# Kernel optimization log

Hardware: AMD Instinct MI355X
Metric: run time of the kernel (lower is better)

Reference implementation:

```python
import jax, jax.numpy as jnp
import numpy as np

B, S, K = 256, 50, 8
D, NH, NL = 512, 8, 2
N_KNOWS, N_PROBS = 1000, 20000
L2 = 2 * NL  # forward layers then backward layers, stacked
HD = D // NH
NEG = -1e9


def _ln(x, g, b, eps=1e-5):
    mu = x.mean(-1, keepdims=True)
    v = ((x - mu) ** 2).mean(-1, keepdims=True)
    return (x - mu) * jax.lax.rsqrt(v + eps) * g + b


def _block(x, m, Wq, bq, Wk, bk, Wv, bv, g1, be1, W1, b1, W2, b2, g2, be2):
    # x: [3B,S,D], m: [3B,1,S,S] additive-OR mask (True = blocked)
    Bx, Sx, Dx = x.shape
    Q = (x @ Wq + bq).reshape(Bx, Sx, NH, HD)
    Kt = (x @ Wk + bk).reshape(Bx, Sx, NH, HD)
    V = (x @ Wv + bv).reshape(Bx, Sx, NH, HD)
    a = jnp.einsum('bqnh,bknh->bnqk', Q, Kt) * (HD ** -0.5)
    a = jnp.where(m, NEG, a)
    p = jax.nn.softmax(a, axis=-1)
    p = jnp.where(m, 0.0, p)  # masked_fill + softmax + where, as in torch source
    o = jnp.einsum('bnqk,bknh->bqnh', p, V).reshape(Bx, Sx, Dx)
    x = _ln(x + o, g1, be1)
    h = jnp.maximum(x @ W1 + b1, 0.0) @ W2 + b2
    return _ln(x + h, g2, be2)


def _forward(probs_his, knows_his, corrs_his, knows_tab, probs_tab, types_tab, pos_tab,
             Wq, bq, Wk, bk, Wv, bv, g1, be1, W1, b1, W2, b2, g2, be2,
             pW1, pb1, pW2, pb2, pW3, pb3):
    info = knows_tab[knows_his].sum(-2) + probs_tab[probs_his] + pos_tab[jnp.arange(S)][None]
    c = corrs_his
    right_t = jnp.where(c, 1, 2)   # corrs==False -> 2
    wrong_t = jnp.where(c, 2, 0)   # corrs==True  -> 2
    norm_t = c.astype(jnp.int32)
    # fold the 3 counterfactual passes (right / wrong / normal) into the batch dim
    x3 = jnp.concatenate([info + types_tab[right_t], info + types_tab[wrong_t], info + types_tab[norm_t]], 0)
    kpm = jnp.tile(probs_his == 0, (3, 1))               # key padding mask [3B,S]
    km = kpm[:, :, None] | kpm[:, None, :]               # OR-combined [3B,S,S]
    tri = jnp.triu(jnp.ones((S, S), bool), 1)
    fm = (tri[None] | km)[:, None]                       # forward (causal) mask
    bm = (tri.T[None] | km)[:, None]                     # backward (anti-causal) mask
    f = x3
    b = x3
    for i in range(NL):
        f = _block(f, fm, Wq[i], bq[i], Wk[i], bk[i], Wv[i], bv[i], g1[i], be1[i], W1[i], b1[i], W2[i], b2[i], g2[i], be2[i])
    for i in range(NL, L2):
        b = _block(b, bm, Wq[i], bq[i], Wk[i], bk[i], Wv[i], bv[i], g1[i], be1[i], W1[i], b1[i], W2[i], b2[i], g2[i], be2[i])
    out = jnp.concatenate([b[:, :1], f[:, :-2] + b[:, 2:], f[:, -1:]], 1)
    h = jnp.concatenate([out, jnp.tile(info, (3, 1, 1))], -1)
    h = jnp.maximum(h @ pW1 + pb1, 0.0)
    h = jnp.maximum(h @ pW2 + pb2, 0.0)
    sc = jax.nn.sigmoid((h @ pW3 + pb3)[..., 0]).reshape(3, B, S)
    # zero out padded positions instead of ragged boolean gather (fixed shape, jit-safe)
    return jnp.where((probs_his > 0)[None], sc, 0.0)


def setup_inputs() -> dict:
    key = jax.random.key(0)
    ks = jax.random.split(key, 16)
    sc = 0.02
    d = {}
    d['probs_his'] = jax.random.randint(ks[0], (B, S), 0, N_PROBS)
    d['knows_his'] = jax.random.randint(ks[1], (B, S, K), 0, N_KNOWS + 1)
    d['corrs_his'] = jax.random.randint(ks[2], (B, S), 0, 2).astype(bool)
    d['knows_tab'] = (jax.random.normal(ks[3], (N_KNOWS + 1, D)) * sc).at[0].set(0.0)  # padding_idx=0
    d['probs_tab'] = (jax.random.normal(ks[4], (N_PROBS + 1, D)) * sc).at[0].set(0.0)
    d['types_tab'] = jax.random.normal(ks[5], (3, D)) * sc
    d['pos_tab'] = jax.random.normal(ks[6], (50, D)) * sc
    d['Wq'] = jax.random.normal(ks[7], (L2, D, D)) * sc
    d['Wk'] = jax.random.normal(ks[8], (L2, D, D)) * sc
    d['Wv'] = jax.random.normal(ks[9], (L2, D, D)) * sc
    d['W1'] = jax.random.normal(ks[10], (L2, D, D)) * sc
    d['W2'] = jax.random.normal(ks[11], (L2, D, D)) * sc
    for n in ('bq', 'bk', 'bv', 'b1', 'b2', 'be1', 'be2'):
        d[n] = jnp.zeros((L2, D))
    d['g1'] = jnp.ones((L2, D))
    d['g2'] = jnp.ones((L2, D))
    d['pW1'] = jax.random.normal(ks[12], (2 * D, D)) * sc
    d['pb1'] = jnp.zeros((D,))
    d['pW2'] = jax.random.normal(ks[13], (D, D // 2)) * sc
    d['pb2'] = jnp.zeros((D // 2,))
    d['pW3'] = jax.random.normal(ks[14], (D // 2, 1)) * sc
    d['pb3'] = jnp.zeros((1,))
    return d


def reference(probs_his, knows_his, corrs_his, knows_tab, probs_tab, types_tab, pos_tab,
              Wq, bq, Wk, bk, Wv, bv, g1, be1, W1, b1, W2, b2, g2, be2,
              pW1, pb1, pW2, pb2, pW3, pb3):
    return _forward(probs_his, knows_his, corrs_his, knows_tab, probs_tab, types_tab, pos_tab,
                    Wq, bq, Wk, bk, Wv, bv, g1, be1, W1, b1, W2, b2, g2, be2,
                    pW1, pb1, pW2, pb2, pW3, pb3)
```

## Files before the change

kernel.cpp:

```cpp
#include <hip/hip_runtime.h>
#include <hip/hip_bf16.h>

#define SEQ 50
#define DD  512
#define NHD 8
#define HDIM 64
#define MPROWS 38400
#define MTROWS 76800

typedef __hip_bfloat16 bf;
typedef __attribute__((ext_vector_type(8))) short bf16x8;
typedef __attribute__((ext_vector_type(4))) float f32x4;

__device__ __forceinline__ float bf2f(unsigned short u) {
    unsigned int x = ((unsigned int)u) << 16;
    return __builtin_bit_cast(float, x);
}
__device__ __forceinline__ unsigned short f2bu(float f) {
    unsigned int u = __builtin_bit_cast(unsigned int, f);
    u += 0x7fffu + ((u >> 16) & 1u);
    return (unsigned short)(u >> 16);
}

#define ASYNC16(g, l) __builtin_amdgcn_global_load_lds( \
    (__attribute__((address_space(1))) void*)(g),       \
    (__attribute__((address_space(3))) void*)(l), 16, 0, 0)

__global__ __launch_bounds__(256) void transpose_cast(
    const float* __restrict__ src, bf* __restrict__ dst,
    int R, int C, size_t sStride, size_t dStride)
{
    __shared__ float tile[32][33];
    int l = blockIdx.z;
    src += (size_t)l * sStride;
    dst += (size_t)l * dStride;
    int c0 = blockIdx.x * 32, r0 = blockIdx.y * 32;
    int tx = threadIdx.x & 31, ty = threadIdx.x >> 5;
    for (int i = ty; i < 32; i += 8)
        tile[i][tx] = src[(size_t)(r0 + i) * C + c0 + tx];
    __syncthreads();
    for (int i = ty; i < 32; i += 8)
        dst[(size_t)(c0 + i) * R + r0 + tx] = __float2bfloat16(tile[tx][i]);
}

__global__ __launch_bounds__(256) void biascat_kernel(
    const float* __restrict__ bq, const float* __restrict__ bk,
    const float* __restrict__ bv, float* __restrict__ out)
{
    int i = blockIdx.x * 256 + threadIdx.x;
    if (i >= 4 * 1536) return;
    int l = i / 1536, c = i % 1536;
    float v;
    if (c < 512)       v = bq[l * 512 + c];
    else if (c < 1024) v = bk[l * 512 + c - 512];
    else               v = bv[l * 512 + c - 1024];
    out[i] = v;
}

__global__ __launch_bounds__(256) void tproj_kernel(
    const float* __restrict__ types_tab, const bf* __restrict__ WTqkv,
    bf* __restrict__ Tt)
{
    int gid = blockIdx.x * 256 + threadIdx.x;
    if (gid >= 9216) return;
    int hl = gid / 4608;
    int t  = (gid / 1536) % 3;
    int n  = gid % 1536;
    const unsigned short* w =
        (const unsigned short*)(WTqkv + (size_t)(hl * 2) * 786432 + (size_t)n * 512);
    const float* ty = types_tab + t * 512;
    float a = 0.f;
    for (int k = 0; k < 512; ++k) a += ty[k] * bf2f(w[k]);
    Tt[gid] = __float2bfloat16(a);
}

__global__ __launch_bounds__(256) void embed_kernel(
    const int* __restrict__ probs_his, const int* __restrict__ knows_his,
    const int* __restrict__ corrs, const float* __restrict__ knows_tab,
    const float* __restrict__ probs_tab, const float* __restrict__ types_tab,
    const float* __restrict__ pos_tab, bf* __restrict__ info, bf* __restrict__ X)
{
    int bs = blockIdx.x * 4 + (threadIdx.x >> 6);
    int lane = threadIdx.x & 63;
    int s = bs % SEQ;
    int p = probs_his[bs];
    int c = corrs[bs];
    int d0 = lane * 8;

    float v[8];
    #pragma unroll
    for (int j = 0; j < 8; ++j)
        v[j] = probs_tab[(size_t)p * DD + d0 + j] + pos_tab[(size_t)s * DD + d0 + j];
    for (int k = 0; k < 8; ++k) {
        int ki = knows_his[bs * 8 + k];
        const float* kr = knows_tab + (size_t)ki * DD + d0;
        #pragma unroll
        for (int j = 0; j < 8; ++j) v[j] += kr[j];
    }
    int t0 = c ? 1 : 2;
    int t1 = c ? 2 : 0;
    int t2 = c ? 1 : 0;
    const float* T0 = types_tab + t0 * DD + d0;
    const float* T1 = types_tab + t1 * DD + d0;
    const float* T2 = types_tab + t2 * DD + d0;
    uint4 xi, x0, x1, x2;
    unsigned short* pi = (unsigned short*)&xi;
    unsigned short* p0 = (unsigned short*)&x0;
    unsigned short* p1 = (unsigned short*)&x1;
    unsigned short* p2 = (unsigned short*)&x2;
    #pragma unroll
    for (int j = 0; j < 8; ++j) {
        pi[j] = f2bu(v[j]);
        p0[j] = f2bu(v[j] + T0[j]);
        p1[j] = f2bu(v[j] + T1[j]);
        p2[j] = f2bu(v[j] + T2[j]);
    }
    size_t base = (size_t)bs * DD + d0;
    const size_t PB = (size_t)12800 * DD;
    *(uint4*)(info + base) = xi;
    *(uint4*)(X + 0 * PB + base) = x0;
    *(uint4*)(X + 1 * PB + base) = x1;
    *(uint4*)(X + 2 * PB + base) = x2;
    *(uint4*)(X + 3 * PB + base) = x0;
    *(uint4*)(X + 4 * PB + base) = x1;
    *(uint4*)(X + 5 * PB + base) = x2;
}

template <int RELU>
__global__ __launch_bounds__(256) void gemm_bt(
    const bf* __restrict__ Ap, const bf* __restrict__ WT0, const bf* __restrict__ WT1,
    const float* __restrict__ bias0, const float* __restrict__ bias1,
    bf* __restrict__ Cp, int N, int Kd, int nN, int mtHalf)
{
    __shared__ bf Al[128 * 64];
    __shared__ bf Bl[128 * 64];
    int nwg = gridDim.x;
    int f = blockIdx.x;
    int q8 = nwg >> 3, r8 = nwg & 7;
    int xcd = f & 7, pos = f >> 3;
    int e = (xcd < r8 ? xcd * (q8 + 1) : r8 * (q8 + 1) + (xcd - r8) * q8) + pos;
    int bm = e / nN, bn = e - bm * nN;
    const bf* WTp;
    const float* bias;
    if (bm < mtHalf) { WTp = WT0; bias = bias0; }
    else             { WTp = WT1; bias = bias1; }
    int m0 = bm * 128, n0 = bn * 128;
    int t = threadIdx.x, lane = t & 63, wave = t >> 6;
    int wr = wave >> 1, wc = wave & 1;
    int lr = lane & 15, lg = lane >> 4;

    f32x4 acc[4][4];
    #pragma unroll
    for (int m = 0; m < 4; ++m)
        #pragma unroll
        for (int n = 0; n < 4; ++n)
            acc[m][n] = (f32x4){0.f, 0.f, 0.f, 0.f};

    for (int kt = 0; kt < Kd; kt += 64) {
        #pragma unroll
        for (int i = 0; i < 4; ++i) {
            int c = i * 256 + t;
            int row = c >> 3, col = (c & 7) * 8;
            ASYNC16(Ap  + (size_t)(m0 + row) * Kd + kt + col, Al + c * 8);
            ASYNC16(WTp + (size_t)(n0 + row) * Kd + kt + col, Bl + c * 8);
        }
        __syncthreads();
        #pragma unroll
        for (int kk = 0; kk < 64; kk += 32) {
            int ko = kk + lg * 8;
            bf16x8 af[4], bfr[4];
            #pragma unroll
            for (int m = 0; m < 4; ++m)
                af[m] = *(const bf16x8*)(Al + (wr * 64 + m * 16 + lr) * 64 + ko);
            #pragma unroll
            for (int n = 0; n < 4; ++n)
                bfr[n] = *(const bf16x8*)(Bl + (wc * 64 + n * 16 + lr) * 64 + ko);
            #pragma unroll
            for (int m = 0; m < 4; ++m)
                #pragma unroll
                for (int n = 0; n < 4; ++n)
                    acc[m][n] = __builtin_amdgcn_mfma_f32_16x16x32_bf16(af[m], bfr[n], acc[m][n], 0, 0, 0);
        }
        __syncthreads();
    }
    unsigned short* Cs = (unsigned short*)Cp;
    #pragma unroll
    for (int n = 0; n < 4; ++n) {
        int col = n0 + wc * 64 + n * 16 + lr;
        float bvv = bias[col];
        #pragma unroll
        for (int m = 0; m < 4; ++m) {
            #pragma unroll
            for (int r = 0; r < 4; ++r) {
                int row = m0 + wr * 64 + m * 16 + lg * 4 + r;
                float v = acc[m][n][r] + bvv;
                if (RELU) v = fmaxf(v, 0.f);
                Cs[(size_t)row * N + col] = f2bu(v);
            }
        }
    }
}

template <int RELU>
__global__ __launch_bounds__(512, 2) void gemm8(
    const bf* __restrict__ Ap, const bf* __restrict__ WTp,
    const float* __restrict__ bias, bf* __restrict__ Cp,
    int N, int Kd, int nN)
{
    __shared__ __align__(16) bf As[2][16384];
    __shared__ __align__(16) bf Bs[2][16384];

    int nwg = gridDim.x, f = blockIdx.x;
    int q8 = nwg >> 3, r8 = nwg & 7;
    int xcd = f & 7, pos = f >> 3;
    int e = (xcd < r8 ? xcd * (q8 + 1) : r8 * (q8 + 1) + (xcd - r8) * q8) + pos;
    int bm = e / nN, bn = e - bm * nN;
    int m0 = bm * 256, n0 = bn * 256;
    int t = threadIdx.x, lane = t & 63, wave = t >> 6;
    int wm = wave >> 2, wn = wave & 3;
    int lr = lane & 15, kg = lane >> 4;

    int srow = t >> 3;
    int scolb = (t & 7) * 16;
    const bf* Abase = Ap + (size_t)m0 * Kd;
    const bf* Bbase = WTp + (size_t)n0 * Kd;

#define STG(dsts, base, half, kt) do {                                        \
    _Pragma("unroll")                                                         \
    for (int _i = 0; _i < 2; ++_i) {                                          \
        int _r = (half) * 128 + _i * 64 + srow;                               \
        ASYNC16((base) + (size_t)_r * Kd + (kt) +                             \
                    ((scolb ^ ((_r & 7) << 4)) >> 1),                         \
                (dsts) + _r * 64 + (t & 7) * 8);                              \
    } } while (0)

    f32x4 acc[8][4];
    #pragma unroll
    for (int m = 0; m < 8; ++m)
        #pragma unroll
        for (int n = 0; n < 4; ++n)
            acc[m][n] = (f32x4){0.f, 0.f, 0.f, 0.f};

    STG(As[0], Abase, 0, 0);
    STG(As[0], Abase, 1, 0);
    STG(Bs[0], Bbase, 0, 0);
    STG(Bs[0], Bbase, 1, 0);

    int ntile = Kd >> 6;
    bf16x8 breg[4][2];
    for (int j = 0; j < ntile; ++j) {
        int d = j & 1;
        const char* Ab = (const char*)As[d];
        const char* Bb = (const char*)Bs[d];
        asm volatile("s_waitcnt vmcnt(0)" ::: "memory");
        __builtin_amdgcn_s_barrier();
        int kt1 = (j + 1) << 6;
        int pf = (j + 1 < ntile);
        #pragma unroll
        for (int q = 0; q < 4; ++q) {
            if (q == 0) {
                #pragma unroll
                for (int ns = 0; ns < 4; ++ns) {
                    int row = wn * 64 + ns * 16 + lr;
                    int sw = (row & 7) << 4;
                    breg[ns][0] = *(const bf16x8*)(Bb + row * 128 + ((kg * 16) ^ sw));
                    breg[ns][1] = *(const bf16x8*)(Bb + row * 128 + ((64 + kg * 16) ^ sw));
                }
            }
            bf16x8 areg[2][2];
            #pragma unroll
            for (int mm = 0; mm < 2; ++mm) {
                int row = wm * 128 + (2 * q + mm) * 16 + lr;
                int sw = (row & 7) << 4;
                areg[mm][0] = *(const bf16x8*)(Ab + row * 128 + ((kg * 16) ^ sw));
                areg[mm][1] = *(const bf16x8*)(Ab + row * 128 + ((64 + kg * 16) ^ sw));
            }
            if (pf) {
                if (q == 0)      STG(As[d ^ 1], Abase, 0, kt1);
                else if (q == 1) STG(As[d ^ 1], Abase, 1, kt1);
                else if (q == 2) STG(Bs[d ^ 1], Bbase, 0, kt1);
                else             STG(Bs[d ^ 1], Bbase, 1, kt1);
            }
            __builtin_amdgcn_s_barrier();
            __builtin_amdgcn_s_setprio(1);
            #pragma unroll
            for (int mm = 0; mm < 2; ++mm)
                #pragma unroll
                for (int ns = 0; ns < 4; ++ns) {
                    acc[2 * q + mm][ns] = __builtin_amdgcn_mfma_f32_16x16x32_bf16(
                        areg[mm][0], breg[ns][0], acc[2 * q + mm][ns], 0, 0, 0);
                    acc[2 * q + mm][ns] = __builtin_amdgcn_mfma_f32_16x16x32_bf16(
                        areg[mm][1], breg[ns][1], acc[2 * q + mm][ns], 0, 0, 0);
                }
            __builtin_amdgcn_s_setprio(0);
            if (q != 3) __builtin_amdgcn_s_barrier();
        }
    }
#undef STG

    unsigned short* Cs = (unsigned short*)Cp;
    #pragma unroll
    for (int ns = 0; ns < 4; ++ns) {
        int col = n0 + wn * 64 + ns * 16 + lr;
        float bvv = bias[col];
        #pragma unroll
        for (int ms = 0; ms < 8; ++ms) {
            #pragma unroll
            for (int rr = 0; rr < 4; ++rr) {
                int row = m0 + wm * 128 + ms * 16 + kg * 4 + rr;
                float v = acc[ms][ns][rr] + bvv;
                if (RELU) v = fmaxf(v, 0.f);
                Cs[(size_t)row * N + col] = f2bu(v);
            }
        }
    }
}

__global__ __launch_bounds__(256) void gemm_l0(
    const bf* __restrict__ Ap, const bf* __restrict__ WTp,
    const float* __restrict__ bias, const bf* __restrict__ Tth,
    const int* __restrict__ corrs, bf* __restrict__ QKVc)
{
    __shared__ bf Al[128 * 64];
    __shared__ bf Bl[128 * 64];
    const int nN = 12, Kd = 512, N = 1536;
    int nwg = gridDim.x;
    int f = blockIdx.x;
    int q8 = nwg >> 3, r8 = nwg & 7;
    int xcd = f & 7, pos = f >> 3;
    int e = (xcd < r8 ? xcd * (q8 + 1) : r8 * (q8 + 1) + (xcd - r8) * q8) + pos;
    int bm = e / nN, bn = e - bm * nN;
    int m0 = bm * 128, n0 = bn * 128;
    int t = threadIdx.x, lane = t & 63, wave = t >> 6;
    int wr = wave >> 1, wc = wave & 1;
    int lr = lane & 15, lg = lane >> 4;

    f32x4 acc[4][4];
    #pragma unroll
    for (int m = 0; m < 4; ++m)
        #pragma unroll
        for (int n = 0; n < 4; ++n)
            acc[m][n] = (f32x4){0.f, 0.f, 0.f, 0.f};

    for (int kt = 0; kt < Kd; kt += 64) {
        #pragma unroll
        for (int i = 0; i < 4; ++i) {
            int c = i * 256 + t;
            int row = c >> 3, col = (c & 7) * 8;
            ASYNC16(Ap  + (size_t)(m0 + row) * Kd + kt + col, Al + c * 8);
            ASYNC16(WTp + (size_t)(n0 + row) * Kd + kt + col, Bl + c * 8);
        }
        __syncthreads();
        #pragma unroll
        for (int kk = 0; kk < 64; kk += 32) {
            int ko = kk + lg * 8;
            bf16x8 af[4], bfr[4];
            #pragma unroll
            for (int m = 0; m < 4; ++m)
                af[m] = *(const bf16x8*)(Al + (wr * 64 + m * 16 + lr) * 64 + ko);
            #pragma unroll
            for (int n = 0; n < 4; ++n)
                bfr[n] = *(const bf16x8*)(Bl + (wc * 64 + n * 16 + lr) * 64 + ko);
            #pragma unroll
            for (int m = 0; m < 4; ++m)
                #pragma unroll
                for (int n = 0; n < 4; ++n)
                    acc[m][n] = __builtin_amdgcn_mfma_f32_16x16x32_bf16(af[m], bfr[n], acc[m][n], 0, 0, 0);
        }
        __syncthreads();
    }
    unsigned short* Cs = (unsigned short*)QKVc;
    const unsigned short* Tu = (const unsigned short*)Tth;
    #pragma unroll
    for (int n = 0; n < 4; ++n) {
        int col = n0 + wc * 64 + n * 16 + lr;
        float bvv = bias[col];
        float T0c = bf2f(Tu[0 * 1536 + col]);
        float T1c = bf2f(Tu[1 * 1536 + col]);
        float T2c = bf2f(Tu[2 * 1536 + col]);
        #pragma unroll
        for (int m = 0; m < 4; ++m) {
            #pragma unroll
            for (int r = 0; r < 4; ++r) {
                int row = m0 + wr * 64 + m * 16 + lg * 4 + r;
                int c = corrs[row];
                float v = acc[m][n][r] + bvv;
                float tv0 = c ? T1c : T2c;
                float tv1 = c ? T2c : T0c;
                float tv2 = c ? T1c : T0c;
                size_t b0 = (size_t)row * N + col;
                Cs[b0]                     = f2bu(v + tv0);
                Cs[b0 + (size_t)12800 * N] = f2bu(v + tv1);
                Cs[b0 + (size_t)25600 * N] = f2bu(v + tv2);
            }
        }
    }
}

__global__ __launch_bounds__(256) void gemm_head(
    const bf* __restrict__ Ap, const bf* __restrict__ WTp,
    const bf* __restrict__ IPp, bf* __restrict__ Cp, int nN)
{
    __shared__ bf Al[128 * 64];
    __shared__ bf Bl[128 * 64];
    const int Kd = 512, N = 512;
    int nwg = gridDim.x;
    int f = blockIdx.x;
    int q8 = nwg >> 3, r8 = nwg & 7;
    int xcd = f & 7, pos = f >> 3;
    int e = (xcd < r8 ? xcd * (q8 + 1) : r8 * (q8 + 1) + (xcd - r8) * q8) + pos;
    int bm = e / nN, bn = e - bm * nN;
    int m0 = bm * 128, n0 = bn * 128;
    int t = threadIdx.x, lane = t & 63, wave = t >> 6;
    int wr = wave >> 1, wc = wave & 1;
    int lr = lane & 15, lg = lane >> 4;

    f32x4 acc[4][4];
    #pragma unroll
    for (int m = 0; m < 4; ++m)
        #pragma unroll
        for (int n = 0; n < 4; ++n)
            acc[m][n] = (f32x4){0.f, 0.f, 0.f, 0.f};

    for (int kt = 0; kt < Kd; kt += 64) {
        #pragma unroll
        for (int i = 0; i < 4; ++i) {
            int c = i * 256 + t;
            int row = c >> 3, col = (c & 7) * 8;
            ASYNC16(Ap  + (size_t)(m0 + row) * Kd + kt + col, Al + c * 8);
            ASYNC16(WTp + (size_t)(n0 + row) * Kd + kt + col, Bl + c * 8);
        }
        __syncthreads();
        #pragma unroll
        for (int kk = 0; kk < 64; kk += 32) {
            int ko = kk + lg * 8;
            bf16x8 af[4], bfr[4];
            #pragma unroll
            for (int m = 0; m < 4; ++m)
                af[m] = *(const bf16x8*)(Al + (wr * 64 + m * 16 + lr) * 64 + ko);
            #pragma unroll
            for (int n = 0; n < 4; ++n)
                bfr[n] = *(const bf16x8*)(Bl + (wc * 64 + n * 16 + lr) * 64 + ko);
            #pragma unroll
            for (int m = 0; m < 4; ++m)
                #pragma unroll
                for (int n = 0; n < 4; ++n)
                    acc[m][n] = __builtin_amdgcn_mfma_f32_16x16x32_bf16(af[m], bfr[n], acc[m][n], 0, 0, 0);
        }
        __syncthreads();
    }
    unsigned short* Cs = (unsigned short*)Cp;
    const unsigned short* IPu = (const unsigned short*)IPp;
    #pragma unroll
    for (int n = 0; n < 4; ++n) {
        int col = n0 + wc * 64 + n * 16 + lr;
        #pragma unroll
        for (int m = 0; m < 4; ++m) {
            #pragma unroll
            for (int r = 0; r < 4; ++r) {
                int row = m0 + wr * 64 + m * 16 + lg * 4 + r;
                int rr = row % 12800;
                float v = acc[m][n][r] + bf2f(IPu[(size_t)rr * 512 + col]);
                v = fmaxf(v, 0.f);
                Cs[(size_t)row * N + col] = f2bu(v);
            }
        }
    }
}

__global__ __launch_bounds__(128, 2) void attn_mfma(
    const bf* __restrict__ QKVc, const int* __restrict__ probs_his,
    bf* __restrict__ Oc, int seq0)
{
    __shared__ bf Pl_s[2][4096];
    __shared__ bf Vt_s[2][4096];
    int wave = threadIdx.x >> 6, lane = threadIdx.x & 63;
    bf* Pl = Pl_s[wave];
    bf* Vt = Vt_s[wave];
    int task = blockIdx.x * 2 + wave;
    int h = task & 7, seqL = task >> 3;
    int seqG = seq0 + seqL;
    int st = seqG / 768, b = seqG % 256;
    int lr = lane & 15, kg = lane >> 4;
    const bf* Qb = QKVc + (size_t)seqL * SEQ * 1536 + h * HDIM;
    const bf* Kb = Qb + 512;
    const bf* Vb = Qb + 1024;

    int pvv = (lane < SEQ) ? probs_his[b * SEQ + lane] : 1;
    unsigned long long padm = __ballot(pvv == 0) | 0xFFFC000000000000ull;

    #pragma unroll
    for (int it = 0; it < 8; ++it) {
        int idx = it * 64 + lane;
        int key = idx >> 3, d0 = (idx & 7) * 8;
        uint4 v4 = make_uint4(0u, 0u, 0u, 0u);
        if (key < SEQ) v4 = *(const uint4*)(Vb + (size_t)key * 1536 + d0);
        unsigned short* vs = (unsigned short*)&v4;
        #pragma unroll
        for (int j = 0; j < 8; ++j) {
            int d = d0 + j;
            int byt = (d * 128 + key * 2) ^ ((j & 7) << 4);
            *(unsigned short*)((char*)Vt + byt) = vs[j];
        }
    }

    bf16x8 kf[4][2], qf[4][2];
    #pragma unroll
    for (int m = 0; m < 4; ++m) {
        int rk = 16 * m + lr; if (rk > SEQ - 1) rk = SEQ - 1;
        #pragma unroll
        for (int kb = 0; kb < 2; ++kb) {
            kf[m][kb] = *(const bf16x8*)(Kb + (size_t)rk * 1536 + kb * 32 + kg * 8);
            qf[m][kb] = *(const bf16x8*)(Qb + (size_t)rk * 1536 + kb * 32 + kg * 8);
        }
    }
    f32x4 sacc[4][4];
    #pragma unroll
    for (int m = 0; m < 4; ++m)
        #pragma unroll
        for (int n = 0; n < 4; ++n)
            sacc[m][n] = (f32x4){0.f, 0.f, 0.f, 0.f};
    #pragma unroll
    for (int kb = 0; kb < 2; ++kb)
        #pragma unroll
        for (int m = 0; m < 4; ++m)
            #pragma unroll
            for (int n = 0; n < 4; ++n)
                sacc[m][n] = __builtin_amdgcn_mfma_f32_16x16x32_bf16(kf[m][kb], qf[n][kb], sacc[m][n], 0, 0, 0);

    #pragma unroll
    for (int n = 0; n < 4; ++n) {
        int q = 16 * n + lr;
        int qpad = (int)((padm >> q) & 1ull);
        float p[4][4];
        float mx = -3e38f;
        #pragma unroll
        for (int m = 0; m < 4; ++m)
            #pragma unroll
            for (int r = 0; r < 4; ++r) {
                int key = 16 * m + 4 * kg + r;
                int blocked = qpad | (int)((padm >> key) & 1ull) |
                              (st == 0 ? (key > q) : (key < q));
                float s = sacc[m][n][r] * 0.125f;
                p[m][r] = blocked ? -3e38f : s;
                if (!blocked) mx = fmaxf(mx, s);
            }
        mx = fmaxf(mx, __shfl_xor(mx, 16));
        mx = fmaxf(mx, __shfl_xor(mx, 32));
        float sum = 0.f;
        #pragma unroll
        for (int m = 0; m < 4; ++m)
            #pragma unroll
            for (int r = 0; r < 4; ++r) {
                float e = (p[m][r] > -1e37f) ? __expf(p[m][r] - mx) : 0.f;
                p[m][r] = e;
                sum += e;
            }
        sum += __shfl_xor(sum, 16);
        sum += __shfl_xor(sum, 32);
        float inv = (sum > 0.f) ? 1.f / sum : 0.f;
        #pragma unroll
        for (int m = 0; m < 4; ++m) {
            unsigned int u0 = (unsigned int)f2bu(p[m][0] * inv) |
                              ((unsigned int)f2bu(p[m][1] * inv) << 16);
            unsigned int u1 = (unsigned int)f2bu(p[m][2] * inv) |
                              ((unsigned int)f2bu(p[m][3] * inv) << 16);
            int base = (q * 128 + (16 * m + 4 * kg) * 2) ^ ((q & 7) << 4);
            *(unsigned int*)((char*)Pl + base) = u0;
            *(unsigned int*)((char*)Pl + base + 4) = u1;
        }
    }

    f32x4 oacc[4][4];
    #pragma unroll
    for (int m = 0; m < 4; ++m)
        #pragma unroll
        for (int n = 0; n < 4; ++n)
            oacc[m][n] = (f32x4){0.f, 0.f, 0.f, 0.f};
    #pragma unroll
    for (int kb = 0; kb < 2; ++kb) {
        bf16x8 vf[4], pf[4];
        #pragma unroll
        for (int m = 0; m < 4; ++m) {
            int row = 16 * m + lr;
            int byt = (row * 128 + (kb * 32 + kg * 8) * 2) ^ ((row & 7) << 4);
            vf[m] = *(const bf16x8*)((char*)Vt + byt);
            pf[m] = *(const bf16x8*)((char*)Pl + byt);
        }
        #pragma unroll
        for (int m = 0; m < 4; ++m)
            #pragma unroll
            for (int n = 0; n < 4; ++n)
                oacc[m][n] = __builtin_amdgcn_mfma_f32_16x16x32_bf16(vf[m], pf[n], oacc[m][n], 0, 0, 0);
    }
    #pragma unroll
    for (int n = 0; n < 4; ++n) {
        int q = 16 * n + lr;
        if (q < SEQ) {
            #pragma unroll
            for (int m = 0; m < 4; ++m) {
                uint2 ov;
                ov.x = (unsigned int)f2bu(oacc[m][n][0]) | ((unsigned int)f2bu(oacc[m][n][1]) << 16);
                ov.y = (unsigned int)f2bu(oacc[m][n][2]) | ((unsigned int)f2bu(oacc[m][n][3]) << 16);
                *(uint2*)(Oc + (size_t)(seqL * SEQ + q) * DD + h * HDIM + 16 * m + 4 * kg) = ov;
            }
        }
    }
}

__global__ __launch_bounds__(256) void ln_kernel(
    bf* __restrict__ X, const bf* __restrict__ Rb,
    const float* __restrict__ g_all, const float* __restrict__ be_all,
    int lf, int lb)
{
    int row = blockIdx.x * 4 + (threadIdx.x >> 6);
    int lane = threadIdx.x & 63;
    int layer = (row < MPROWS) ? lf : lb;
    const float* g = g_all + layer * DD;
    const float* be = be_all + layer * DD;
    uint4 xa = *((const uint4*)(X + (size_t)row * DD) + lane);
    uint4 ra = *((const uint4*)(Rb + (size_t)row * DD) + lane);
    unsigned short* xs = (unsigned short*)&xa;
    unsigned short* rs = (unsigned short*)&ra;
    float v[8];
    float sum = 0.f;
    #pragma unroll
    for (int j = 0; j < 8; ++j) { v[j] = bf2f(xs[j]) + bf2f(rs[j]); sum += v[j]; }
    #pragma unroll
    for (int o = 1; o < 64; o <<= 1) sum += __shfl_xor(sum, o);
    float mu = sum * (1.f / 512.f);
    float ss = 0.f;
    #pragma unroll
    for (int j = 0; j < 8; ++j) { float d = v[j] - mu; ss += d * d; }
    #pragma unroll
    for (int o = 1; o < 64; o <<= 1) ss += __shfl_xor(ss, o);
    float inv = rsqrtf(ss * (1.f / 512.f) + 1e-5f);
    int d0 = lane * 8;
    uint4 ov;
    unsigned short* os = (unsigned short*)&ov;
    #pragma unroll
    for (int j = 0; j < 8; ++j)
        os[j] = f2bu((v[j] - mu) * inv * g[d0 + j] + be[d0 + j]);
    *((uint4*)(X + (size_t)row * DD) + lane) = ov;
}

__global__ __launch_bounds__(256) void combine_kernel(
    const bf* __restrict__ X, const bf* __restrict__ info,
    bf* __restrict__ Hinc, int rh0, int hstride, int withInfo)
{
    int rl = blockIdx.x * 4 + (threadIdx.x >> 6);
    int rh = rh0 + rl;
    int lane = threadIdx.x & 63;
    int s = rh % SEQ, pb = rh / SEQ, b = pb & 255;
    const size_t MPD = (size_t)MPROWS * DD;
    uint4 o;
    if (s == 0) {
        o = *((const uint4*)(X + MPD + (size_t)(pb * SEQ) * DD) + lane);
    } else if (s == SEQ - 1) {
        o = *((const uint4*)(X + (size_t)(pb * SEQ + SEQ - 1) * DD) + lane);
    } else {
        uint4 a = *((const uint4*)(X + (size_t)(pb * SEQ + s - 1) * DD) + lane);
        uint4 c2 = *((const uint4*)(X + MPD + (size_t)(pb * SEQ + s + 1) * DD) + lane);
        unsigned short* as = (unsigned short*)&a;
        unsigned short* cs = (unsigned short*)&c2;
        unsigned short* os = (unsigned short*)&o;
        #pragma unroll
        for (int j = 0; j < 8; ++j) os[j] = f2bu(bf2f(as[j]) + bf2f(cs[j]));
    }
    *((uint4*)(Hinc + (size_t)rl * hstride) + lane) = o;
    if (withInfo) {
        uint4 iv = *((const uint4*)(info + (size_t)(b * SEQ + s) * DD) + lane);
        *((uint4*)(Hinc + (size_t)rl * hstride + 512) + lane) = iv;
    }
}

__global__ __launch_bounds__(256) void head_final(
    const bf* __restrict__ h2c, const float* __restrict__ pW3,
    const float* __restrict__ pb3, const int* __restrict__ probs_his,
    float* __restrict__ out, int rh0)
{
    int rl = blockIdx.x * 4 + (threadIdx.x >> 6);
    int row = rh0 + rl;
    int lane = threadIdx.x & 63;
    uint2 hv = *((const uint2*)(h2c + (size_t)rl * 256) + lane);
    unsigned short* hs = (unsigned short*)&hv;
    float s = 0.f;
    #pragma unroll
    for (int j = 0; j < 4; ++j) s += bf2f(hs[j]) * pW3[lane * 4 + j];
    #pragma unroll
    for (int o = 1; o < 64; o <<= 1) s += __shfl_xor(s, o);
    if (lane == 0) {
        float logit = s + pb3[0];
        float sc = 1.f / (1.f + __expf(-logit));
        int bb = (row / SEQ) & 255, ss2 = row % SEQ;
        out[row] = (probs_his[bb * SEQ + ss2] > 0) ? sc : 0.f;
    }
}

extern "C" void kernel_launch(void* const* d_in, const int* in_sizes, int n_in,
                              void* d_out, int out_size, void* d_ws, size_t ws_size,
                              hipStream_t stream) {
    const int*   probs_his = (const int*)d_in[0];
    const int*   knows_his = (const int*)d_in[1];
    const int*   corrs     = (const int*)d_in[2];
    const float* knows_tab = (const float*)d_in[3];
    const float* probs_tab = (const float*)d_in[4];
    const float* types_tab = (const float*)d_in[5];
    const float* pos_tab   = (const float*)d_in[6];
    const float* Wq = (const float*)d_in[7];
    const float* Wk = (const float*)d_in[8];
    const float* Wv = (const float*)d_in[9];
    const float* W1 = (const float*)d_in[10];
    const float* W2 = (const float*)d_in[11];
    const float* bq = (const float*)d_in[12];
    const float* bk = (const float*)d_in[13];
    const float* bv = (const float*)d_in[14];
    const float* b1 = (const float*)d_in[15];
    const float* b2 = (const float*)d_in[16];
    const float* be1 = (const float*)d_in[17];
    const float* be2 = (const float*)d_in[18];
    const float* g1 = (const float*)d_in[19];
    const float* g2 = (const float*)d_in[20];
    const float* pW1 = (const float*)d_in[21];
    const float* pb1 = (const float*)d_in[22];
    const float* pW2 = (const float*)d_in[23];
    const float* pb2 = (const float*)d_in[24];
    const float* pW3 = (const float*)d_in[25];
    const float* pb3 = (const float*)d_in[26];

    char* ws = (char*)d_ws;
    bf* WTqkv = (bf*)(ws + 0);
    bf* WT1   = (bf*)(ws + 6291456);
    bf* WT2   = (bf*)(ws + 8388608);
    bf* pW1T  = (bf*)(ws + 10485760);
    bf* pW1aT = (bf*)(ws + 11534336);
    bf* pW1bT = (bf*)(ws + 12058624);
    bf* pW2T  = (bf*)(ws + 12582912);
    float* bqkv = (float*)(ws + 12845056);
    bf* info  = (bf*)(ws + 12869632);
    bf* X     = (bf*)(ws + 25976832);
    const size_t FIXED = 104620032ull;
    const size_t FULLSCR = (size_t)38400 * 4096;

    int CR;
    if      (ws_size >= FIXED + FULLSCR)                  CR = 38400;
    else if (ws_size >= FIXED + (size_t)19200 * 4096)     CR = 19200;
    else if (ws_size >= FIXED + (size_t)9600  * 4096)     CR = 9600;
    else                                                  CR = 3200;
    const int full = (CR == 38400) &&
        (ws_size >= FIXED + FULLSCR + 18432);
    bf* Tt = (bf*)(ws + FIXED + FULLSCR);

    char* SCR = ws + FIXED;

    biascat_kernel<<<dim3(24), dim3(256), 0, stream>>>(bq, bk, bv, bqkv);
    transpose_cast<<<dim3(16,16,4), dim3(256), 0, stream>>>(Wq, WTqkv,          512, 512, 262144, 786432);
    transpose_cast<<<dim3(16,16,4), dim3(256), 0, stream>>>(Wk, WTqkv + 262144, 512, 512, 262144, 786432);
    transpose_cast<<<dim3(16,16,4), dim3(256), 0, stream>>>(Wv, WTqkv + 524288, 512, 512, 262144, 786432);
    transpose_cast<<<dim3(16,16,4), dim3(256), 0, stream>>>(W1, WT1, 512, 512, 262144, 262144);
    transpose_cast<<<dim3(16,16,4), dim3(256), 0, stream>>>(W2, WT2, 512, 512, 262144, 262144);
    transpose_cast<<<dim3(16,32,1), dim3(256), 0, stream>>>(pW1, pW1T, 1024, 512, 0, 0);
    transpose_cast<<<dim3(16,16,1), dim3(256), 0, stream>>>(pW1, pW1aT, 512, 512, 0, 0);
    transpose_cast<<<dim3(16,16,1), dim3(256), 0, stream>>>(pW1 + 262144, pW1bT, 512, 512, 0, 0);
    transpose_cast<<<dim3(8,16,1),  dim3(256), 0, stream>>>(pW2, pW2T, 512, 256, 0, 0);
    embed_kernel<<<dim3(3200), dim3(256), 0, stream>>>(probs_his, knows_his, corrs,
        knows_tab, probs_tab, types_tab, pos_tab, info, X);
    if (full)
        tproj_kernel<<<dim3(36), dim3(256), 0, stream>>>(types_tab, WTqkv, Tt);

    const int BIG = 1 << 30;

    if (full) {
        bf* QKVc = (bf*)SCR;
        bf* Oc   = (bf*)(SCR + (size_t)38400 * 3072);
        bf* F1c  = (bf*)SCR;
        bf* F2c  = (bf*)(SCR + (size_t)76800 * 1024);
        bf* Hin  = (bf*)SCR;
        bf* h1c  = (bf*)(SCR + 39321600);
        bf* h2c  = (bf*)(SCR + 78643200);
        bf* IPb  = (bf*)(SCR + 98304000);

        for (int i = 0; i < 2; ++i) {
            for (int hlf = 0; hlf < 2; ++hlf) {
                int lidx = i + 2 * hlf;
                bf* Xh = X + (size_t)hlf * 38400 * DD;
                if (i == 0) {
                    gemm_l0<<<dim3(1200), dim3(256), 0, stream>>>(
                        info, WTqkv + (size_t)lidx * 786432, bqkv + lidx * 1536,
                        Tt + hlf * 4608, corrs, QKVc);
                } else {
                    gemm8<0><<<dim3(900), dim3(512), 0, stream>>>(
                        Xh, WTqkv + (size_t)lidx * 786432, bqkv + lidx * 1536,
                        QKVc, 1536, 512, 6);
                }
                attn_mfma<<<dim3(3072), dim3(128), 0, stream>>>(
                    QKVc, probs_his, Oc, hlf * 768);
                ln_kernel<<<dim3(9600), dim3(256), 0, stream>>>(
                    Xh, Oc, g1, be1, lidx, lidx);
            }
            gemm_bt<1><<<dim3(2400), dim3(256), 0, stream>>>(
                X, WT1 + (size_t)i * 262144, WT1 + (size_t)(i + 2) * 262144,
                b1 + i * 512, b1 + (i + 2) * 512, F1c, 512, 512, 4, 300);
            gemm_bt<0><<<dim3(2400), dim3(256), 0, stream>>>(
                F1c, WT2 + (size_t)i * 262144, WT2 + (size_t)(i + 2) * 262144,
                b2 + i * 512, b2 + (i + 2) * 512, F2c, 512, 512, 4, 300);
            ln_kernel<<<dim3(19200), dim3(256), 0, stream>>>(
                X, F2c, g2, be2, i, i + 2);
        }

        combine_kernel<<<dim3(9600), dim3(256), 0, stream>>>(X, info, Hin, 0, 512, 0);
        gemm_bt<0><<<dim3(400), dim3(256), 0, stream>>>(
            info, pW1bT, pW1bT, pb1, pb1, IPb, 512, 512, 4, BIG);
        gemm_head<<<dim3(1200), dim3(256), 0, stream>>>(Hin, pW1aT, IPb, h1c, 4);
        gemm_bt<1><<<dim3(600), dim3(256), 0, stream>>>(
            h1c, pW2T, pW2T, pb2, pb2, h2c, 256, 512, 2, BIG);
        head_final<<<dim3(9600), dim3(256), 0, stream>>>(
            h2c, pW3, pb3, probs_his, (float*)d_out, 0);
        return;
    }

    bf* QKVc = (bf*)SCR;
    bf* Oc   = (bf*)(SCR + (size_t)CR * 3072);
    bf* F1c  = (bf*)SCR;
    bf* F2c  = (bf*)(SCR + (size_t)CR * 1024);
    bf* Hinc = (bf*)SCR;
    bf* h1c  = (bf*)(SCR + (size_t)CR * 2048);
    bf* h2c  = (bf*)(SCR + (size_t)CR * 3072);

    const int nck = 38400 / CR;
    const int MT = CR / 128;
    for (int i = 0; i < 2; ++i) {
        for (int hlf = 0; hlf < 2; ++hlf) {
            int lidx = i + 2 * hlf;
            const bf* WTq  = WTqkv + (size_t)lidx * 786432;
            const bf* WT1l = WT1   + (size_t)lidx * 262144;
            const bf* WT2l = WT2   + (size_t)lidx * 262144;
            for (int c = 0; c < nck; ++c) {
                int r0 = hlf * 38400 + c * CR;
                gemm_bt<0><<<dim3(MT * 12), dim3(256), 0, stream>>>(
                    X + (size_t)r0 * DD, WTq, WTq, bqkv + lidx * 1536,
                    bqkv + lidx * 1536, QKVc, 1536, 512, 12, BIG);
                attn_mfma<<<dim3((CR/50) * 4), dim3(128), 0, stream>>>(
                    QKVc, probs_his, Oc, r0 / 50);
                ln_kernel<<<dim3(CR/4), dim3(256), 0, stream>>>(
                    X + (size_t)r0 * DD, Oc, g1, be1, lidx, lidx);
            }
            for (int c = 0; c < nck; ++c) {
                int r0 = hlf * 38400 + c * CR;
                gemm_bt<1><<<dim3(MT * 4), dim3(256), 0, stream>>>(
                    X + (size_t)r0 * DD, WT1l, WT1l, b1 + lidx * 512,
                    b1 + lidx * 512, F1c, 512, 512, 4, BIG);
                gemm_bt<0><<<dim3(MT * 4), dim3(256), 0, stream>>>(
                    F1c, WT2l, WT2l, b2 + lidx * 512, b2 + lidx * 512,
                    F2c, 512, 512, 4, BIG);
                ln_kernel<<<dim3(CR/4), dim3(256), 0, stream>>>(
                    X + (size_t)r0 * DD, F2c, g2, be2, lidx, lidx);
            }
        }
    }
    for (int c = 0; c < nck; ++c) {
        int rh0 = c * CR;
        combine_kernel<<<dim3(CR/4), dim3(256), 0, stream>>>(X, info, Hinc, rh0, 1024, 1);
        gemm_bt<1><<<dim3(MT * 4), dim3(256), 0, stream>>>(
            Hinc, pW1T, pW1T, pb1, pb1, h1c, 512, 1024, 4, BIG);
        gemm_bt<1><<<dim3(MT * 2), dim3(256), 0, stream>>>(
            h1c, pW2T, pW2T, pb2, pb2, h2c, 256, 512, 2, BIG);
        head_final<<<dim3(CR/4), dim3(256), 0, stream>>>(
            h2c, pW3, pb3, probs_his, (float*)d_out, rh0);
    }
}
```

Before: 1.123 ms.

## Compute layer-0 QKV once per base row and apply type offsets in attention

The layer-0 QKV projection now runs on the 12800 base rows only, through the large-tile gemm8 kernel. The per-pass type-embedding projection (selected by corrs) is added to Q, K and V inside a templated attention kernel, instead of writing three counterfactual copies from a dedicated GEMM. The FFN GEMMs move from gemm_bt to gemm8, which gains dual weight/bias selection per row half. The gemm8 epilogue stages its output tile through swizzled LDS so that global stores become coalesced 16-byte writes. Adding the offset after the GEMM changes bf16 rounding slightly, and it adds per-element conversion work and corrs lookups inside attention.

```diff
diff --git a/kernel.cpp b/kernel.cpp
--- a/kernel.cpp
+++ b/kernel.cpp
@@ -203,9 +203,9 @@
 
 template <int RELU>
 __global__ __launch_bounds__(512, 2) void gemm8(
-    const bf* __restrict__ Ap, const bf* __restrict__ WTp,
-    const float* __restrict__ bias, bf* __restrict__ Cp,
-    int N, int Kd, int nN)
+    const bf* __restrict__ Ap, const bf* __restrict__ WT0, const bf* __restrict__ WT1,
+    const float* __restrict__ bias0, const float* __restrict__ bias1,
+    bf* __restrict__ Cp, int N, int Kd, int nN, int mtHalf)
 {
     __shared__ __align__(16) bf As[2][16384];
     __shared__ __align__(16) bf Bs[2][16384];
@@ -215,6 +215,10 @@
     int xcd = f & 7, pos = f >> 3;
     int e = (xcd < r8 ? xcd * (q8 + 1) : r8 * (q8 + 1) + (xcd - r8) * q8) + pos;
     int bm = e / nN, bn = e - bm * nN;
+    const bf* WTp;
+    const float* bias;
+    if (bm < mtHalf) { WTp = WT0; bias = bias0; }
+    else             { WTp = WT1; bias = bias1; }
     int m0 = bm * 256, n0 = bn * 256;
     int t = threadIdx.x, lane = t & 63, wave = t >> 6;
     int wm = wave >> 2, wn = wave & 3;
@@ -298,101 +302,39 @@
     }
 #undef STG
 
-    unsigned short* Cs = (unsigned short*)Cp;
-    #pragma unroll
-    for (int ns = 0; ns < 4; ++ns) {
-        int col = n0 + wn * 64 + ns * 16 + lr;
-        float bvv = bias[col];
-        #pragma unroll
-        for (int ms = 0; ms < 8; ++ms) {
-            #pragma unroll
-            for (int rr = 0; rr < 4; ++rr) {
-                int row = m0 + wm * 128 + ms * 16 + kg * 4 + rr;
-                float v = acc[ms][ns][rr] + bvv;
-                if (RELU) v = fmaxf(v, 0.f);
-                Cs[(size_t)row * N + col] = f2bu(v);
-            }
-        }
-    }
-}
-
-__global__ __launch_bounds__(256) void gemm_l0(
-    const bf* __restrict__ Ap, const bf* __restrict__ WTp,
-    const float* __restrict__ bias, const bf* __restrict__ Tth,
-    const int* __restrict__ corrs, bf* __restrict__ QKVc)
-{
-    __shared__ bf Al[128 * 64];
-    __shared__ bf Bl[128 * 64];
-    const int nN = 12, Kd = 512, N = 1536;
-    int nwg = gridDim.x;
-    int f = blockIdx.x;
-    int q8 = nwg >> 3, r8 = nwg & 7;
-    int xcd = f & 7, pos = f >> 3;
-    int e = (xcd < r8 ? xcd * (q8 + 1) : r8 * (q8 + 1) + (xcd - r8) * q8) + pos;
-    int bm = e / nN, bn = e - bm * nN;
-    int m0 = bm * 128, n0 = bn * 128;
-    int t = threadIdx.x, lane = t & 63, wave = t >> 6;
-    int wr = wave >> 1, wc = wave & 1;
-    int lr = lane & 15, lg = lane >> 4;
-
-    f32x4 acc[4][4];
-    #pragma unroll
-    for (int m = 0; m < 4; ++m)
-        #pragma unroll
-        for (int n = 0; n < 4; ++n)
-            acc[m][n] = (f32x4){0.f, 0.f, 0.f, 0.f};
-
-    for (int kt = 0; kt < Kd; kt += 64) {
-        #pragma unroll
-        for (int i = 0; i < 4; ++i) {
-            int c = i * 256 + t;
-            int row = c >> 3, col = (c & 7) * 8;
-            ASYNC16(Ap  + (size_t)(m0 + row) * Kd + kt + col, Al + c * 8);
-            ASYNC16(WTp + (size_t)(n0 + row) * Kd + kt + col, Bl + c * 8);
-        }
-        __syncthreads();
-        #pragma unroll
-        for (int kk = 0; kk < 64; kk += 32) {
-            int ko = kk + lg * 8;
-            bf16x8 af[4], bfr[4];
-            #pragma unroll
-            for (int m = 0; m < 4; ++m)
-                af[m] = *(const bf16x8*)(Al + (wr * 64 + m * 16 + lr) * 64 + ko);
-            #pragma unroll
-            for (int n = 0; n < 4; ++n)
-                bfr[n] = *(const bf16x8*)(Bl + (wc * 64 + n * 16 + lr) * 64 + ko);
-            #pragma unroll
-            for (int m = 0; m < 4; ++m)
+    __syncthreads();
+    {
+        char* base = (wm == 0) ? (char*)&As[0][0] : (char*)&Bs[0][0];
+        #pragma unroll
+        for (int ns = 0; ns < 4; ++ns) {
+            int col = wn * 64 + ns * 16 + lr;
+            float bvv = bias[n0 + col];
+            #pragma unroll
+            for (int ms = 0; ms < 8; ++ms) {
                 #pragma unroll
-                for (int n = 0; n < 4; ++n)
-                    acc[m][n] = __builtin_amdgcn_mfma_f32_16x16x32_bf16(af[m], bfr[n], acc[m][n], 0, 0, 0);
-        }
-        __syncthreads();
-    }
-    unsigned short* Cs = (unsigned short*)QKVc;
-    const unsigned short* Tu = (const unsigned short*)Tth;
-    #pragma unroll
-    for (int n = 0; n < 4; ++n) {
-        int col = n0 + wc * 64 + n * 16 + lr;
-        float bvv = bias[col];
-        float T0c = bf2f(Tu[0 * 1536 + col]);
-        float T1c = bf2f(Tu[1 * 1536 + col]);
-        float T2c = bf2f(Tu[2 * 1536 + col]);
-        #pragma unroll
-        for (int m = 0; m < 4; ++m) {
-            #pragma unroll
-            for (int r = 0; r < 4; ++r) {
-                int row = m0 + wr * 64 + m * 16 + lg * 4 + r;
-                int c = corrs[row];
-                float v = acc[m][n][r] + bvv;
-                float tv0 = c ? T1c : T2c;
-                float tv1 = c ? T2c : T0c;
-                float tv2 = c ? T1c : T0c;
-                size_t b0 = (size_t)row * N + col;
-                Cs[b0]                     = f2bu(v + tv0);
-                Cs[b0 + (size_t)12800 * N] = f2bu(v + tv1);
-                Cs[b0 + (size_t)25600 * N] = f2bu(v + tv2);
-            }
+                for (int rr = 0; rr < 4; ++rr) {
+                    int r128 = ms * 16 + kg * 4 + rr;
+                    float v = acc[ms][ns][rr] + bvv;
+                    if (RELU) v = fmaxf(v, 0.f);
+                    *(unsigned short*)(base + r128 * 512 +
+                        ((col * 2) ^ ((r128 & 7) << 4))) = f2bu(v);
+                }
+            }
+        }
+    }
+    __syncthreads();
+    {
+        unsigned short* Cs = (unsigned short*)Cp;
+        int row = t >> 1, hb = (t & 1) * 256;
+        int r128 = row & 127;
+        const char* src = (row < 128) ? (const char*)&As[0][0] : (const char*)&Bs[0][0];
+        char* Crow = (char*)(Cs + (size_t)(m0 + row) * N + n0);
+        int sw = (r128 & 7) << 4;
+        #pragma unroll
+        for (int i2 = 0; i2 < 16; ++i2) {
+            int cb = hb + i2 * 16;
+            uint4 v = *(const uint4*)(src + r128 * 512 + (cb ^ sw));
+            *(uint4*)(Crow + cb) = v;
         }
     }
 }
@@ -468,9 +410,11 @@
     }
 }
 
+template <int L0>
 __global__ __launch_bounds__(128, 2) void attn_mfma(
     const bf* __restrict__ QKVc, const int* __restrict__ probs_his,
-    bf* __restrict__ Oc, int seq0)
+    bf* __restrict__ Oc, int seq0,
+    const bf* __restrict__ Tsel, const int* __restrict__ corrs)
 {
     __shared__ bf Pl_s[2][4096];
     __shared__ bf Vt_s[2][4096];
@@ -481,10 +425,13 @@
     int h = task & 7, seqL = task >> 3;
     int seqG = seq0 + seqL;
     int st = seqG / 768, b = seqG % 256;
+    int pass = (seqG % 768) / 256;
     int lr = lane & 15, kg = lane >> 4;
-    const bf* Qb = QKVc + (size_t)seqL * SEQ * 1536 + h * HDIM;
+    size_t qkrow = L0 ? (size_t)b * SEQ : (size_t)seqL * SEQ;
+    const bf* Qb = QKVc + qkrow * 1536 + h * HDIM;
     const bf* Kb = Qb + 512;
     const bf* Vb = Qb + 1024;
+    const unsigned short* Tu = (const unsigned short*)Tsel;
 
     int pvv = (lane < SEQ) ? probs_his[b * SEQ + lane] : 1;
     unsigned long long padm = __ballot(pvv == 0) | 0xFFFC000000000000ull;
@@ -496,6 +443,15 @@
         uint4 v4 = make_uint4(0u, 0u, 0u, 0u);
         if (key < SEQ) v4 = *(const uint4*)(Vb + (size_t)key * 1536 + d0);
         unsigned short* vs = (unsigned short*)&v4;
+        if (L0) {
+            int kk2 = (key < SEQ) ? key : (SEQ - 1);
+            int cc = corrs[b * SEQ + kk2];
+            int tt = (pass == 0) ? (cc ? 1 : 2) : (pass == 1) ? (cc ? 2 : 0) : (cc ? 1 : 0);
+            const unsigned short* Tv = Tu + tt * 1536 + 1024 + h * HDIM + d0;
+            #pragma unroll
+            for (int j = 0; j < 8; ++j)
+                vs[j] = f2bu(bf2f(vs[j]) + bf2f(Tv[j]));
+        }
         #pragma unroll
         for (int j = 0; j < 8; ++j) {
             int d = d0 + j;
@@ -508,10 +464,23 @@
     #pragma unroll
     for (int m = 0; m < 4; ++m) {
         int rk = 16 * m + lr; if (rk > SEQ - 1) rk = SEQ - 1;
+        int tt = 0;
+        if (L0) {
+            int cc = corrs[b * SEQ + rk];
+            tt = (pass == 0) ? (cc ? 1 : 2) : (pass == 1) ? (cc ? 2 : 0) : (cc ? 1 : 0);
+        }
         #pragma unroll
         for (int kb = 0; kb < 2; ++kb) {
             kf[m][kb] = *(const bf16x8*)(Kb + (size_t)rk * 1536 + kb * 32 + kg * 8);
             qf[m][kb] = *(const bf16x8*)(Qb + (size_t)rk * 1536 + kb * 32 + kg * 8);
+            if (L0) {
+                const unsigned short* Tq = Tu + tt * 1536 + h * HDIM + kb * 32 + kg * 8;
+                #pragma unroll
+                for (int j = 0; j < 8; ++j) {
+                    qf[m][kb][j] = (short)f2bu(bf2f((unsigned short)qf[m][kb][j]) + bf2f(Tq[j]));
+                    kf[m][kb][j] = (short)f2bu(bf2f((unsigned short)kf[m][kb][j]) + bf2f(Tq[512 + j]));
+                }
+            }
         }
     }
     f32x4 sacc[4][4];
@@ -784,26 +753,29 @@
             for (int hlf = 0; hlf < 2; ++hlf) {
                 int lidx = i + 2 * hlf;
                 bf* Xh = X + (size_t)hlf * 38400 * DD;
+                const bf* WTq = WTqkv + (size_t)lidx * 786432;
                 if (i == 0) {
-                    gemm_l0<<<dim3(1200), dim3(256), 0, stream>>>(
-                        info, WTqkv + (size_t)lidx * 786432, bqkv + lidx * 1536,
-                        Tt + hlf * 4608, corrs, QKVc);
+                    gemm8<0><<<dim3(300), dim3(512), 0, stream>>>(
+                        info, WTq, WTq, bqkv + lidx * 1536, bqkv + lidx * 1536,
+                        QKVc, 1536, 512, 6, BIG);
+                    attn_mfma<1><<<dim3(3072), dim3(128), 0, stream>>>(
+                        QKVc, probs_his, Oc, hlf * 768, Tt + hlf * 4608, corrs);
                 } else {
                     gemm8<0><<<dim3(900), dim3(512), 0, stream>>>(
-                        Xh, WTqkv + (size_t)lidx * 786432, bqkv + lidx * 1536,
-                        QKVc, 1536, 512, 6);
+                        Xh, WTq, WTq, bqkv + lidx * 1536, bqkv + lidx * 1536,
+                        QKVc, 1536, 512, 6, BIG);
+                    attn_mfma<0><<<dim3(3072), dim3(128), 0, stream>>>(
+                        QKVc, probs_his, Oc, hlf * 768, nullptr, nullptr);
                 }
-                attn_mfma<<<dim3(3072), dim3(128), 0, stream>>>(
-                    QKVc, probs_his, Oc, hlf * 768);
                 ln_kernel<<<dim3(9600), dim3(256), 0, stream>>>(
                     Xh, Oc, g1, be1, lidx, lidx);
             }
-            gemm_bt<1><<<dim3(2400), dim3(256), 0, stream>>>(
+            gemm8<1><<<dim3(600), dim3(512), 0, stream>>>(
                 X, WT1 + (size_t)i * 262144, WT1 + (size_t)(i + 2) * 262144,
-                b1 + i * 512, b1 + (i + 2) * 512, F1c, 512, 512, 4, 300);
-            gemm_bt<0><<<dim3(2400), dim3(256), 0, stream>>>(
+                b1 + i * 512, b1 + (i + 2) * 512, F1c, 512, 512, 2, 150);
+            gemm8<0><<<dim3(600), dim3(512), 0, stream>>>(
                 F1c, WT2 + (size_t)i * 262144, WT2 + (size_t)(i + 2) * 262144,
-                b2 + i * 512, b2 + (i + 2) * 512, F2c, 512, 512, 4, 300);
+                b2 + i * 512, b2 + (i + 2) * 512, F2c, 512, 512, 2, 150);
             ln_kernel<<<dim3(19200), dim3(256), 0, stream>>>(
                 X, F2c, g2, be2, i, i + 2);
         }
@@ -840,8 +812,8 @@
                 gemm_bt<0><<<dim3(MT * 12), dim3(256), 0, stream>>>(
                     X + (size_t)r0 * DD, WTq, WTq, bqkv + lidx * 1536,
                     bqkv + lidx * 1536, QKVc, 1536, 512, 12, BIG);
-                attn_mfma<<<dim3((CR/50) * 4), dim3(128), 0, stream>>>(
-                    QKVc, probs_his, Oc, r0 / 50);
+                attn_mfma<0><<<dim3((CR/50) * 4), dim3(128), 0, stream>>>(
+                    QKVc, probs_his, Oc, r0 / 50, nullptr, nullptr);
                 ln_kernel<<<dim3(CR/4), dim3(256), 0, stream>>>(
                     X + (size_t)r0 * DD, Oc, g1, be1, lidx, lidx);
             }
```

Result: slower. 1.183 ms (+5.3%).
